# Performance work log

Measured on AMD Instinct MI355X. Metric: run time of the kernel, lower is better.

The kernel has to match this reference:

```python
import jax, jax.numpy as jnp
import numpy as np

N_ORDERS = 2
CHUNK = 64            # real tokens per chunk
LINEAR_ACTIVATION = False
STAB = 10000.0


def _ensure_stability(x):
    x = jnp.clip(x, -STAB, STAB)
    return jnp.nan_to_num(x, nan=0.0, posinf=STAB, neginf=-STAB)


def setup_inputs() -> dict:
    key = jax.random.key(0)
    k1, k2, k3, k4 = jax.random.split(key, 4)
    B, H, NC, D = 2, 16, 32, 128
    CT = CHUNK * N_ORDERS  # 128 virtual tokens per chunk
    s = 1.0 / np.sqrt(D)
    q_chunks = jax.random.normal(k1, (B, H, NC, CT, D), jnp.float32) * s
    W = jax.random.normal(k2, (B, H, NC, CT, D), jnp.float32) * s
    U = jax.random.normal(k3, (B, H, NC, CT, D), jnp.float32) * s
    h0 = jax.random.normal(k4, (B, H, D, D), jnp.float32) * s
    return {"q_chunks": q_chunks, "W": W, "U": U, "h0": h0}


def _gelu_norm(h):
    # h_norm/2 * gelu(2*h/h_norm, tanh) applied to chunk-boundary state
    n = jnp.linalg.norm(h, axis=-1, keepdims=True) + 1e-6
    return n / 2.0 * jax.nn.gelu(2.0 * h / n, approximate=True)


def _delta_product_scan(q_chunks, W, U, h0):
    B, H, NC, CT, D = q_chunks.shape
    C = CT // N_ORDERS

    def body(h, chunk):
        q_c, w_c, u_c = chunk  # each [B,H,CT,D]
        # virtual-token layout: token c, step s lives at index c*n_orders+s
        qs = q_c.reshape(B, H, C, N_ORDERS, D)
        ws = w_c.reshape(B, H, C, N_ORDERS, D)
        us = u_c.reshape(B, H, C, N_ORDERS, D)
        state = jnp.broadcast_to(h[:, :, None], (B, H, C, D, D))  # per-token state
        outs = []
        for step in range(N_ORDERS):
            q_s = qs[:, :, :, step]
            w_s = ws[:, :, :, step]
            u_s = us[:, :, :, step]
            k_trans_h = jnp.einsum('bhcd,bhcde->bhce', w_s, state)
            u_val = u_s - k_trans_h
            o_inter = jnp.einsum('bhcd,bhcde->bhce', q_s, state)
            o_intra = q_s * u_val  # elementwise, as in source
            outs.append(o_intra + o_inter)
            state = _ensure_stability(state + w_s[..., :, None] * u_val[..., None, :])
        out = jnp.stack(outs, axis=3).reshape(B, H, CT, D)
        h_new = state[:, :, -1]
        if not LINEAR_ACTIVATION:
            h_new = _gelu_norm(h_new)
        return h_new, out

    chunks = (jnp.moveaxis(q_chunks, 2, 0), jnp.moveaxis(W, 2, 0), jnp.moveaxis(U, 2, 0))
    h_final, ys = jax.lax.scan(body, h0, chunks)
    return jnp.moveaxis(ys, 0, 2), h_final  # [B,H,NC,CT,D], [B,H,D,D]


def reference(q_chunks, W, U, h0):
    return _delta_product_scan(q_chunks, W, U, h0)
```

## Files before the change

### kernel.cpp

```cpp
#include <hip/hip_runtime.h>


#define Dd 128
#define NCH 32
#define YS 16777216

typedef __attribute__((ext_vector_type(4))) float floatx4;
typedef __attribute__((ext_vector_type(8))) short short8;

__device__ __forceinline__ unsigned short f2bf(float f) {
  unsigned int u = __float_as_uint(f);
  u += 0x7fffu + ((u >> 16) & 1u);
  return (unsigned short)(u >> 16);
}
__device__ __forceinline__ float clampf(float x) {
  return fminf(fmaxf(x, -10000.0f), 10000.0f);
}

__global__ __launch_bounds__(512) void p1_scan(const float* __restrict__ W,
    const float* __restrict__ U, const float* __restrict__ h0,
    unsigned short* __restrict__ hws, float* __restrict__ out) {
  __shared__ float wpre[NCH * 2 * Dd];
  __shared__ float upre[NCH * 2 * Dd];
  __shared__ float d10pre[NCH];
  __shared__ float mvp[2 * 4 * Dd];
  __shared__ float uvs[2 * Dd];
  __shared__ float sqb[Dd * 129];
  __shared__ float psum[Dd * 4];
  __shared__ float nrm2[Dd], nrmh[Dd];

  const int bh = blockIdx.x;
  const int t = threadIdx.x;
  const int e = t & 127, dq = t >> 7;

  {
    const float* Wg = W + (size_t)bh * NCH * 16384;
    const float* Ug = U + (size_t)bh * NCH * 16384;
#pragma unroll
    for (int k = 0; k < 4; k++) {
      int idx4 = k * 512 + t;
      int n = idx4 >> 6;
      int rem = idx4 & 63;
      int r = rem >> 5, e4 = (rem & 31) * 4;
      size_t g = (size_t)n * 16384 + (size_t)(126 + r) * Dd + e4;
      *(float4*)&wpre[idx4 * 4] = *(const float4*)&Wg[g];
      *(float4*)&upre[idx4 * 4] = *(const float4*)&Ug[g];
    }
  }
  {
    const float4* hg = (const float4*)(h0 + (size_t)bh * 16384);
#pragma unroll
    for (int k = 0; k < 8; k++) {
      int idx4 = k * 512 + t;
      float4 v = hg[idx4];
      int d = idx4 >> 5, e4 = (idx4 & 31) * 4;
      sqb[d * 129 + e4 + 0] = v.x;
      sqb[d * 129 + e4 + 1] = v.y;
      sqb[d * 129 + e4 + 2] = v.z;
      sqb[d * 129 + e4 + 3] = v.w;
    }
  }
  __syncthreads();
  {
    int n = t >> 4, j = t & 15;
    const float* w0p = &wpre[n * 256 + 8 * j];
    const float* w1p = &wpre[n * 256 + Dd + 8 * j];
    float p = 0.f;
#pragma unroll
    for (int i = 0; i < 8; i++) p += w0p[i] * w1p[i];
    p += __shfl_xor(p, 1, 64);
    p += __shfl_xor(p, 2, 64);
    p += __shfl_xor(p, 4, 64);
    p += __shfl_xor(p, 8, 64);
    if (j == 0) d10pre[n] = p;
  }
  float hr[32];
#pragma unroll
  for (int i = 0; i < 32; i++) hr[i] = sqb[(dq * 32 + i) * 129 + e];
  __syncthreads();

  unsigned short* hwsb = hws + (size_t)bh * NCH * 16384;
  {
    unsigned int pk[16];
#pragma unroll
    for (int i = 0; i < 16; i++)
      pk[i] = (unsigned)f2bf(hr[2 * i]) | ((unsigned)f2bf(hr[2 * i + 1]) << 16);
    uint4* dst = (uint4*)(hwsb + (size_t)e * Dd + dq * 32);
    dst[0] = make_uint4(pk[0], pk[1], pk[2], pk[3]);
    dst[1] = make_uint4(pk[4], pk[5], pk[6], pk[7]);
    dst[2] = make_uint4(pk[8], pk[9], pk[10], pk[11]);
    dst[3] = make_uint4(pk[12], pk[13], pk[14], pk[15]);
  }

  for (int n = 0; n < NCH; n++) {
    floatx4 w0v[8], w1v[8];
#pragma unroll
    for (int i = 0; i < 8; i++) {
      w0v[i] = *(const floatx4*)&wpre[n * 256 + dq * 32 + 4 * i];
      w1v[i] = *(const floatx4*)&wpre[n * 256 + Dd + dq * 32 + 4 * i];
    }
    float a0 = 0.f, a1 = 0.f;
#pragma unroll
    for (int i = 0; i < 8; i++)
#pragma unroll
      for (int j = 0; j < 4; j++) {
        float h = hr[4 * i + j];
        a0 += w0v[i][j] * h;
        a1 += w1v[i][j] * h;
      }
    mvp[dq * Dd + e] = a0;
    mvp[512 + dq * Dd + e] = a1;
    __syncthreads();
    if (t < Dd) {
      float t0 = mvp[t] + mvp[Dd + t] + mvp[2 * Dd + t] + mvp[3 * Dd + t];
      float t1 = mvp[512 + t] + mvp[512 + Dd + t] + mvp[512 + 2 * Dd + t] +
                 mvp[512 + 3 * Dd + t];
      float u0 = upre[n * 256 + t];
      float u1 = upre[n * 256 + Dd + t];
      float uv0 = u0 - t0;
      float uv1 = u1 - t1 - d10pre[n] * uv0;
      uvs[t] = uv0;
      uvs[Dd + t] = uv1;
    }
    __syncthreads();
    const float uv0 = uvs[e], uv1 = uvs[Dd + e];
#pragma unroll
    for (int i = 0; i < 8; i++)
#pragma unroll
      for (int j = 0; j < 4; j++) {
        int ii = 4 * i + j;
        float s = clampf(clampf(hr[ii] + w0v[i][j] * uv0) + w1v[i][j] * uv1);
        hr[ii] = s;
        sqb[(dq * 32 + ii) * 129 + e] = s;
      }
    __syncthreads();
    {
      const int d2 = t >> 2, eq = t & 3;
      float acc = 0.f;
#pragma unroll
      for (int i = 0; i < 32; i++) {
        int ii = (i + 8 * eq) & 31;
        float v = sqb[d2 * 129 + eq * 32 + ii];
        acc += v * v;
      }
      psum[d2 * 4 + eq] = acc;
    }
    __syncthreads();
    if (t < Dd) {
      floatx4 p = *(const floatx4*)&psum[t * 4];
      float nd = sqrtf(p[0] + p[1] + p[2] + p[3]) + 1e-6f;
      nrm2[t] = 2.0f / nd;
      nrmh[t] = 0.5f * nd;
    }
    __syncthreads();
    floatx4 r2v[8], hnv[8];
#pragma unroll
    for (int i = 0; i < 8; i++) {
      r2v[i] = *(const floatx4*)&nrm2[dq * 32 + 4 * i];
      hnv[i] = *(const floatx4*)&nrmh[dq * 32 + 4 * i];
    }
#pragma unroll
    for (int i = 0; i < 8; i++)
#pragma unroll
      for (int j = 0; j < 4; j++) {
        int ii = 4 * i + j;
        float x = hr[ii] * r2v[i][j];
        float x2 = x * x;
        float aa = x * fmaf(0.071354816f, x2, 1.59576912f);
        float ex = __expf(-aa);
        float g = x / (1.0f + ex);
        hr[ii] = hnv[i][j] * g;
      }
    if (n < NCH - 1) {
      unsigned int pk[16];
#pragma unroll
      for (int i = 0; i < 16; i++)
        pk[i] = (unsigned)f2bf(hr[2 * i]) | ((unsigned)f2bf(hr[2 * i + 1]) << 16);
      uint4* dst = (uint4*)(hwsb + (size_t)(n + 1) * 16384 + (size_t)e * Dd + dq * 32);
      dst[0] = make_uint4(pk[0], pk[1], pk[2], pk[3]);
      dst[1] = make_uint4(pk[4], pk[5], pk[6], pk[7]);
      dst[2] = make_uint4(pk[8], pk[9], pk[10], pk[11]);
      dst[3] = make_uint4(pk[12], pk[13], pk[14], pk[15]);
    } else {
      float* ob = out + YS + (size_t)bh * 16384;
#pragma unroll
      for (int i = 0; i < 32; i++) ob[(dq * 32 + i) * Dd + e] = hr[i];
    }
  }
}

__global__ __launch_bounds__(512) void p2_out(const float* __restrict__ Q,
    const float* __restrict__ W, const float* __restrict__ U,
    const unsigned short* __restrict__ hws, float* __restrict__ out) {
  __shared__ unsigned short hT[Dd * 136];
  __shared__ float d10s[64], dq1s[64];
  __shared__ float dps[512];

  const int bid = blockIdx.x;
  const int n = bid & 31, bh = bid >> 5;
  const size_t base = (size_t)(bh * NCH + n) * 16384;
  const float* Qb = Q + base;
  const float* Wb = W + base;
  const float* Ub = U + base;
  float* Ob = out + base;
  const int t = threadIdx.x;

  {
    const uint4* src = (const uint4*)(hws + base);
#pragma unroll
    for (int i = 0; i < 4; i++) {
      int idx = t + i * 512;
      uint4 v = src[idx];
      int e = idx >> 4, j = idx & 15;
      *(uint4*)&hT[e * 136 + j * 8] = v;
    }
  }
  {
    int which = t >> 8, tt = t & 255;
    int c = tt >> 2, part = tt & 3;
    const float* ar = (which ? Qb : Wb) + (2 * c + 1) * Dd + part * 32;
    const float* w0r = Wb + (2 * c) * Dd + part * 32;
    float s = 0.f;
#pragma unroll
    for (int i = 0; i < 32; i++) s += ar[i] * w0r[i];
    dps[which * 256 + tt] = s;
  }
  __syncthreads();
  if (t < 128) {
    int which = t >> 6, c = t & 63;
    const float* p = dps + which * 256 + c * 4;
    float s = p[0] + p[1] + p[2] + p[3];
    (which ? dq1s : d10s)[c] = s;
  }

  const int wv = t >> 6, l = t & 63;
  const int pr = wv >> 2, eq = wv & 3;
  const int lm = l & 15, lq = l >> 4;

  floatx4 acc[2][4][2];
#pragma unroll
  for (int m = 0; m < 2; m++)
#pragma unroll
    for (int ci = 0; ci < 4; ci++)
#pragma unroll
      for (int j = 0; j < 2; j++) acc[m][ci][j] = (floatx4){0.f, 0.f, 0.f, 0.f};

  for (int kc = 0; kc < 4; kc++) {
    const int k0 = kc * 32;
    short8 bfr[2];
#pragma unroll
    for (int j = 0; j < 2; j++) {
      int ee = (2 * eq + j) * 16 + lm;
      bfr[j] = *(const short8*)&hT[ee * 136 + k0 + 8 * lq];
    }
#pragma unroll
    for (int m = 0; m < 2; m++) {
      const float* X = m ? Wb : Qb;
#pragma unroll
      for (int ci = 0; ci < 4; ci++) {
        int c = ci * 16 + lm;
        const float* row = X + (size_t)(2 * c + pr) * Dd + k0 + 8 * lq;
        float4 f0 = ((const float4*)row)[0];
        float4 f1 = ((const float4*)row)[1];
        union { short8 v; unsigned short u[8]; } af;
        af.u[0] = f2bf(f0.x); af.u[1] = f2bf(f0.y);
        af.u[2] = f2bf(f0.z); af.u[3] = f2bf(f0.w);
        af.u[4] = f2bf(f1.x); af.u[5] = f2bf(f1.y);
        af.u[6] = f2bf(f1.z); af.u[7] = f2bf(f1.w);
        acc[m][ci][0] = __builtin_amdgcn_mfma_f32_16x16x32_bf16(af.v, bfr[0], acc[m][ci][0], 0, 0, 0);
        acc[m][ci][1] = __builtin_amdgcn_mfma_f32_16x16x32_bf16(af.v, bfr[1], acc[m][ci][1], 0, 0, 0);
      }
    }
  }
  __syncthreads();
  float* uv0s = (float*)hT;

  if (pr == 0) {
#pragma unroll
    for (int ci = 0; ci < 4; ci++)
#pragma unroll
      for (int j = 0; j < 2; j++) {
        int ee = (2 * eq + j) * 16 + lm;
#pragma unroll
        for (int r = 0; r < 4; r++) {
          int c = ci * 16 + lq * 4 + r;
          float T0 = acc[1][ci][j][r];
          float Q0h = acc[0][ci][j][r];
          float u0 = Ub[(2 * c) * Dd + ee];
          float q0 = Qb[(2 * c) * Dd + ee];
          float uv0 = u0 - T0;
          uv0s[c * Dd + ee] = uv0;
          Ob[(2 * c) * Dd + ee] = q0 * uv0 + Q0h;
        }
      }
  }
  __syncthreads();
  if (pr == 1) {
#pragma unroll
    for (int ci = 0; ci < 4; ci++)
#pragma unroll
      for (int j = 0; j < 2; j++) {
        int ee = (2 * eq + j) * 16 + lm;
#pragma unroll
        for (int r = 0; r < 4; r++) {
          int c = ci * 16 + lq * 4 + r;
          float T1 = acc[1][ci][j][r];
          float Q1h = acc[0][ci][j][r];
          float u1 = Ub[(2 * c + 1) * Dd + ee];
          float q1 = Qb[(2 * c + 1) * Dd + ee];
          float uv0 = uv0s[c * Dd + ee];
          float uv1 = u1 - T1 - d10s[c] * uv0;
          Ob[(2 * c + 1) * Dd + ee] = q1 * uv1 + Q1h + dq1s[c] * uv0;
        }
      }
  }
}

extern "C" void kernel_launch(void* const* d_in, const int* in_sizes, int n_in,
                              void* d_out, int out_size, void* d_ws, size_t ws_size,
                              hipStream_t stream) {
  const float* Q = (const float*)d_in[0];
  const float* W = (const float*)d_in[1];
  const float* U = (const float*)d_in[2];
  const float* h0 = (const float*)d_in[3];
  float* out = (float*)d_out;
  unsigned short* hws = (unsigned short*)d_ws;

  p1_scan<<<32, 512, 0, stream>>>(W, U, h0, hws, out);
  p2_out<<<1024, 512, 0, stream>>>(Q, W, U, hws, out);
}
```

Baseline: 426.8 us.

## Remap scan threads so matvec reduction uses wave shuffles, cutting barriers

Remaps the serial scan kernel's threads so the four partial dot products for each column sit in one wavefront. They are then reduced with xor shuffles instead of through shared memory, which removes two block barriers per chunk. The norm reduction also moves to shuffles, and the gelu-norm scale is simplified algebraically (hn*x*sigmoid becomes h*sigmoid), which drops another barrier and the nrmh array. It also uses fmed3 for the clamp, fast division, and the packed v_cvt_pk_bf16_f32 instruction for bf16 conversion in both kernels. The packed conversion instruction may round or handle NaN differently from the manual round-to-nearest-even code.

After: 445.6 us. 1.04x slower.

```diff
diff --git a/kernel.cpp b/kernel.cpp
--- a/kernel.cpp
+++ b/kernel.cpp
@@ -8,13 +8,10 @@
 typedef __attribute__((ext_vector_type(4))) float floatx4;
 typedef __attribute__((ext_vector_type(8))) short short8;
 
-__device__ __forceinline__ unsigned short f2bf(float f) {
-  unsigned int u = __float_as_uint(f);
-  u += 0x7fffu + ((u >> 16) & 1u);
-  return (unsigned short)(u >> 16);
-}
-__device__ __forceinline__ float clampf(float x) {
-  return fminf(fmaxf(x, -10000.0f), 10000.0f);
+__device__ __forceinline__ unsigned cvtpk(float lo, float hi) {
+  unsigned r;
+  asm("v_cvt_pk_bf16_f32 %0, %1, %2" : "=v"(r) : "v"(lo), "v"(hi));
+  return r;
 }
 
 __global__ __launch_bounds__(512) void p1_scan(const float* __restrict__ W,
@@ -23,15 +20,14 @@
   __shared__ float wpre[NCH * 2 * Dd];
   __shared__ float upre[NCH * 2 * Dd];
   __shared__ float d10pre[NCH];
-  __shared__ float mvp[2 * 4 * Dd];
-  __shared__ float uvs[2 * Dd];
   __shared__ float sqb[Dd * 129];
-  __shared__ float psum[Dd * 4];
-  __shared__ float nrm2[Dd], nrmh[Dd];
+  __shared__ float nrm2[Dd];
 
   const int bh = blockIdx.x;
   const int t = threadIdx.x;
-  const int e = t & 127, dq = t >> 7;
+  const int w = t >> 6, l = t & 63;
+  const int c = (w << 4) | (l & 15);
+  const int rg = l >> 4;
 
   {
     const float* Wg = W + (size_t)bh * NCH * 16384;
@@ -76,16 +72,19 @@
   }
   float hr[32];
 #pragma unroll
-  for (int i = 0; i < 32; i++) hr[i] = sqb[(dq * 32 + i) * 129 + e];
-  __syncthreads();
+  for (int i = 0; i < 32; i++) hr[i] = sqb[(rg * 32 + i) * 129 + c];
+  __syncthreads();
+
+  const int cpos = (c & 96) | ((c + 8 * rg) & 31);
+  float* sqw = &sqb[rg * 32 * 129 + cpos];
+  const float* sqr = &sqb[(t >> 2) * 129 + (t & 3) * 32];
 
   unsigned short* hwsb = hws + (size_t)bh * NCH * 16384;
   {
-    unsigned int pk[16];
-#pragma unroll
-    for (int i = 0; i < 16; i++)
-      pk[i] = (unsigned)f2bf(hr[2 * i]) | ((unsigned)f2bf(hr[2 * i + 1]) << 16);
-    uint4* dst = (uint4*)(hwsb + (size_t)e * Dd + dq * 32);
+    unsigned pk[16];
+#pragma unroll
+    for (int i = 0; i < 16; i++) pk[i] = cvtpk(hr[2 * i], hr[2 * i + 1]);
+    uint4* dst = (uint4*)(hwsb + (size_t)c * Dd + rg * 32);
     dst[0] = make_uint4(pk[0], pk[1], pk[2], pk[3]);
     dst[1] = make_uint4(pk[4], pk[5], pk[6], pk[7]);
     dst[2] = make_uint4(pk[8], pk[9], pk[10], pk[11]);
@@ -94,89 +93,86 @@
 
   for (int n = 0; n < NCH; n++) {
     floatx4 w0v[8], w1v[8];
+    const float* wb = &wpre[n * 256 + rg * 32];
 #pragma unroll
     for (int i = 0; i < 8; i++) {
-      w0v[i] = *(const floatx4*)&wpre[n * 256 + dq * 32 + 4 * i];
-      w1v[i] = *(const floatx4*)&wpre[n * 256 + Dd + dq * 32 + 4 * i];
-    }
-    float a0 = 0.f, a1 = 0.f;
-#pragma unroll
-    for (int i = 0; i < 8; i++)
+      w0v[i] = *(const floatx4*)&wb[4 * i];
+      w1v[i] = *(const floatx4*)&wb[Dd + 4 * i];
+    }
+    float a0 = 0.f, a1 = 0.f, b0 = 0.f, b1 = 0.f;
+#pragma unroll
+    for (int i = 0; i < 8; i += 2) {
 #pragma unroll
       for (int j = 0; j < 4; j++) {
-        float h = hr[4 * i + j];
-        a0 += w0v[i][j] * h;
-        a1 += w1v[i][j] * h;
-      }
-    mvp[dq * Dd + e] = a0;
-    mvp[512 + dq * Dd + e] = a1;
-    __syncthreads();
-    if (t < Dd) {
-      float t0 = mvp[t] + mvp[Dd + t] + mvp[2 * Dd + t] + mvp[3 * Dd + t];
-      float t1 = mvp[512 + t] + mvp[512 + Dd + t] + mvp[512 + 2 * Dd + t] +
-                 mvp[512 + 3 * Dd + t];
-      float u0 = upre[n * 256 + t];
-      float u1 = upre[n * 256 + Dd + t];
-      float uv0 = u0 - t0;
-      float uv1 = u1 - t1 - d10pre[n] * uv0;
-      uvs[t] = uv0;
-      uvs[Dd + t] = uv1;
-    }
-    __syncthreads();
-    const float uv0 = uvs[e], uv1 = uvs[Dd + e];
+        float h0v = hr[4 * i + j];
+        float h1v = hr[4 * i + 4 + j];
+        a0 = fmaf(w0v[i][j], h0v, a0);
+        a1 = fmaf(w1v[i][j], h0v, a1);
+        b0 = fmaf(w0v[i + 1][j], h1v, b0);
+        b1 = fmaf(w1v[i + 1][j], h1v, b1);
+      }
+    }
+    a0 += b0; a1 += b1;
+    a0 += __shfl_xor(a0, 16, 64);
+    a0 += __shfl_xor(a0, 32, 64);
+    a1 += __shfl_xor(a1, 16, 64);
+    a1 += __shfl_xor(a1, 32, 64);
+    const float u0 = upre[n * 256 + c];
+    const float u1 = upre[n * 256 + Dd + c];
+    const float d10 = d10pre[n];
+    const float uv0 = u0 - a0;
+    const float uv1 = u1 - a1 - d10 * uv0;
 #pragma unroll
     for (int i = 0; i < 8; i++)
 #pragma unroll
       for (int j = 0; j < 4; j++) {
         int ii = 4 * i + j;
-        float s = clampf(clampf(hr[ii] + w0v[i][j] * uv0) + w1v[i][j] * uv1);
+        float s = __builtin_amdgcn_fmed3f(fmaf(w0v[i][j], uv0, hr[ii]),
+                                          -10000.0f, 10000.0f);
+        s = __builtin_amdgcn_fmed3f(fmaf(w1v[i][j], uv1, s),
+                                    -10000.0f, 10000.0f);
         hr[ii] = s;
-        sqb[(dq * 32 + ii) * 129 + e] = s;
+        sqw[ii * 129] = s;
       }
     __syncthreads();
     {
-      const int d2 = t >> 2, eq = t & 3;
-      float acc = 0.f;
-#pragma unroll
-      for (int i = 0; i < 32; i++) {
-        int ii = (i + 8 * eq) & 31;
-        float v = sqb[d2 * 129 + eq * 32 + ii];
-        acc += v * v;
-      }
-      psum[d2 * 4 + eq] = acc;
+      float acc = 0.f, acc2 = 0.f;
+#pragma unroll
+      for (int i = 0; i < 32; i += 2) {
+        float v = sqr[i], v2 = sqr[i + 1];
+        acc = fmaf(v, v, acc);
+        acc2 = fmaf(v2, v2, acc2);
+      }
+      acc += acc2;
+      acc += __shfl_xor(acc, 1, 64);
+      acc += __shfl_xor(acc, 2, 64);
+      if ((t & 3) == 0) {
+        float nd = sqrtf(acc) + 1e-6f;
+        nrm2[t >> 2] = __fdividef(2.0f, nd);
+      }
     }
     __syncthreads();
-    if (t < Dd) {
-      floatx4 p = *(const floatx4*)&psum[t * 4];
-      float nd = sqrtf(p[0] + p[1] + p[2] + p[3]) + 1e-6f;
-      nrm2[t] = 2.0f / nd;
-      nrmh[t] = 0.5f * nd;
-    }
-    __syncthreads();
-    floatx4 r2v[8], hnv[8];
-#pragma unroll
-    for (int i = 0; i < 8; i++) {
-      r2v[i] = *(const floatx4*)&nrm2[dq * 32 + 4 * i];
-      hnv[i] = *(const floatx4*)&nrmh[dq * 32 + 4 * i];
-    }
+    floatx4 r2v[8];
+    const float* nb = &nrm2[rg * 32];
+#pragma unroll
+    for (int i = 0; i < 8; i++) r2v[i] = *(const floatx4*)&nb[4 * i];
 #pragma unroll
     for (int i = 0; i < 8; i++)
 #pragma unroll
       for (int j = 0; j < 4; j++) {
         int ii = 4 * i + j;
-        float x = hr[ii] * r2v[i][j];
+        float h = hr[ii];
+        float x = h * r2v[i][j];
         float x2 = x * x;
         float aa = x * fmaf(0.071354816f, x2, 1.59576912f);
         float ex = __expf(-aa);
-        float g = x / (1.0f + ex);
-        hr[ii] = hnv[i][j] * g;
+        hr[ii] = __fdividef(h, 1.0f + ex);
       }
     if (n < NCH - 1) {
-      unsigned int pk[16];
-#pragma unroll
-      for (int i = 0; i < 16; i++)
-        pk[i] = (unsigned)f2bf(hr[2 * i]) | ((unsigned)f2bf(hr[2 * i + 1]) << 16);
-      uint4* dst = (uint4*)(hwsb + (size_t)(n + 1) * 16384 + (size_t)e * Dd + dq * 32);
+      unsigned pk[16];
+#pragma unroll
+      for (int i = 0; i < 16; i++) pk[i] = cvtpk(hr[2 * i], hr[2 * i + 1]);
+      uint4* dst = (uint4*)(hwsb + (size_t)(n + 1) * 16384 + (size_t)c * Dd + rg * 32);
       dst[0] = make_uint4(pk[0], pk[1], pk[2], pk[3]);
       dst[1] = make_uint4(pk[4], pk[5], pk[6], pk[7]);
       dst[2] = make_uint4(pk[8], pk[9], pk[10], pk[11]);
@@ -184,7 +180,7 @@
     } else {
       float* ob = out + YS + (size_t)bh * 16384;
 #pragma unroll
-      for (int i = 0; i < 32; i++) ob[(dq * 32 + i) * Dd + e] = hr[i];
+      for (int i = 0; i < 32; i++) ob[(rg * 32 + i) * Dd + c] = hr[i];
     }
   }
 }
@@ -217,20 +213,23 @@
   }
   {
     int which = t >> 8, tt = t & 255;
-    int c = tt >> 2, part = tt & 3;
-    const float* ar = (which ? Qb : Wb) + (2 * c + 1) * Dd + part * 32;
-    const float* w0r = Wb + (2 * c) * Dd + part * 32;
+    int cc = tt >> 2, part = tt & 3;
+    const float4* ar = (const float4*)((which ? Qb : Wb) + (2 * cc + 1) * Dd + part * 32);
+    const float4* w0r = (const float4*)(Wb + (2 * cc) * Dd + part * 32);
     float s = 0.f;
 #pragma unroll
-    for (int i = 0; i < 32; i++) s += ar[i] * w0r[i];
+    for (int i = 0; i < 8; i++) {
+      float4 a = ar[i], b = w0r[i];
+      s += a.x * b.x + a.y * b.y + a.z * b.z + a.w * b.w;
+    }
     dps[which * 256 + tt] = s;
   }
   __syncthreads();
   if (t < 128) {
-    int which = t >> 6, c = t & 63;
-    const float* p = dps + which * 256 + c * 4;
+    int which = t >> 6, cc = t & 63;
+    const float* p = dps + which * 256 + cc * 4;
     float s = p[0] + p[1] + p[2] + p[3];
-    (which ? dq1s : d10s)[c] = s;
+    (which ? dq1s : d10s)[cc] = s;
   }
 
   const int wv = t >> 6, l = t & 63;
@@ -258,15 +257,15 @@
       const float* X = m ? Wb : Qb;
 #pragma unroll
       for (int ci = 0; ci < 4; ci++) {
-        int c = ci * 16 + lm;
-        const float* row = X + (size_t)(2 * c + pr) * Dd + k0 + 8 * lq;
+        int cc = ci * 16 + lm;
+        const float* row = X + (size_t)(2 * cc + pr) * Dd + k0 + 8 * lq;
         float4 f0 = ((const float4*)row)[0];
         float4 f1 = ((const float4*)row)[1];
-        union { short8 v; unsigned short u[8]; } af;
-        af.u[0] = f2bf(f0.x); af.u[1] = f2bf(f0.y);
-        af.u[2] = f2bf(f0.z); af.u[3] = f2bf(f0.w);
-        af.u[4] = f2bf(f1.x); af.u[5] = f2bf(f1.y);
-        af.u[6] = f2bf(f1.z); af.u[7] = f2bf(f1.w);
+        union { short8 v; unsigned u[4]; } af;
+        af.u[0] = cvtpk(f0.x, f0.y);
+        af.u[1] = cvtpk(f0.z, f0.w);
+        af.u[2] = cvtpk(f1.x, f1.y);
+        af.u[3] = cvtpk(f1.z, f1.w);
         acc[m][ci][0] = __builtin_amdgcn_mfma_f32_16x16x32_bf16(af.v, bfr[0], acc[m][ci][0], 0, 0, 0);
         acc[m][ci][1] = __builtin_amdgcn_mfma_f32_16x16x32_bf16(af.v, bfr[1], acc[m][ci][1], 0, 0, 0);
       }
@@ -283,14 +282,14 @@
         int ee = (2 * eq + j) * 16 + lm;
 #pragma unroll
         for (int r = 0; r < 4; r++) {
-          int c = ci * 16 + lq * 4 + r;
+          int cc = ci * 16 + lq * 4 + r;
           float T0 = acc[1][ci][j][r];
           float Q0h = acc[0][ci][j][r];
-          float u0 = Ub[(2 * c) * Dd + ee];
-          float q0 = Qb[(2 * c) * Dd + ee];
+          float u0 = Ub[(2 * cc) * Dd + ee];
+          float q0 = Qb[(2 * cc) * Dd + ee];
           float uv0 = u0 - T0;
-          uv0s[c * Dd + ee] = uv0;
-          Ob[(2 * c) * Dd + ee] = q0 * uv0 + Q0h;
+          uv0s[cc * Dd + ee] = uv0;
+          Ob[(2 * cc) * Dd + ee] = q0 * uv0 + Q0h;
         }
       }
   }
@@ -303,14 +302,14 @@
         int ee = (2 * eq + j) * 16 + lm;
 #pragma unroll
         for (int r = 0; r < 4; r++) {
-          int c = ci * 16 + lq * 4 + r;
+          int cc = ci * 16 + lq * 4 + r;
           float T1 = acc[1][ci][j][r];
           float Q1h = acc[0][ci][j][r];
-          float u1 = Ub[(2 * c + 1) * Dd + ee];
-          float q1 = Qb[(2 * c + 1) * Dd + ee];
-          float uv0 = uv0s[c * Dd + ee];
-          float uv1 = u1 - T1 - d10s[c] * uv0;
-          Ob[(2 * c + 1) * Dd + ee] = q1 * uv1 + Q1h + dq1s[c] * uv0;
+          float u1 = Ub[(2 * cc + 1) * Dd + ee];
+          float q1 = Qb[(2 * cc + 1) * Dd + ee];
+          float uv0 = uv0s[cc * Dd + ee];
+          float uv1 = u1 - T1 - d10s[cc] * uv0;
+          Ob[(2 * cc + 1) * Dd + ee] = q1 * uv1 + Q1h + dq1s[cc] * uv0;
         }
       }
   }
```
